# Performance work log

Hardware: AMD Instinct MI355X
Metric: run time of the kernel (lower is better)

## Reference

```python
import jax, jax.numpy as jnp
import numpy as np

D_MODEL = 1024
NUM_HEADS = 16
D_K = D_MODEL // NUM_HEADS
D_FF = 4096
B, S = 16, 512


def setup_inputs() -> dict:
    key = jax.random.key(0)
    ks = jax.random.split(key, 9)
    scale = 1.0 / np.sqrt(D_MODEL)
    inp = {
        "x": jax.random.normal(ks[0], (B, S, D_MODEL), dtype=jnp.float32),
        # attention projections, stored as [in, out] (apply as x @ W)
        "Wq": jax.random.normal(ks[1], (D_MODEL, D_MODEL), dtype=jnp.float32) * scale,
        "Wk": jax.random.normal(ks[2], (D_MODEL, D_MODEL), dtype=jnp.float32) * scale,
        "Wv": jax.random.normal(ks[3], (D_MODEL, D_MODEL), dtype=jnp.float32) * scale,
        "Wo": jax.random.normal(ks[4], (D_MODEL, D_MODEL), dtype=jnp.float32) * scale,
        # FFN
        "W1": jax.random.normal(ks[5], (D_MODEL, D_FF), dtype=jnp.float32) * scale,
        "b1": jnp.zeros((D_FF,), dtype=jnp.float32),
        "W2": jax.random.normal(ks[6], (D_FF, D_MODEL), dtype=jnp.float32) * (1.0 / np.sqrt(D_FF)),
        "b2": jnp.zeros((D_MODEL,), dtype=jnp.float32),
        # LayerNorms
        "g1": jnp.ones((D_MODEL,), dtype=jnp.float32),
        "be1": jnp.zeros((D_MODEL,), dtype=jnp.float32),
        "g2": jnp.ones((D_MODEL,), dtype=jnp.float32),
        "be2": jnp.zeros((D_MODEL,), dtype=jnp.float32),
    }
    return inp


def _layernorm(x, g, b, eps=1e-5):
    mu = jnp.mean(x, axis=-1, keepdims=True)
    var = jnp.mean(jnp.square(x - mu), axis=-1, keepdims=True)
    return (x - mu) * jax.lax.rsqrt(var + eps) * g + b


def _mha(x, Wq, Wk, Wv, Wo):
    b, s, _ = x.shape
    def split(h):  # [b,s,d] -> [b,H,s,dk]
        return h.reshape(b, s, NUM_HEADS, D_K).transpose(0, 2, 1, 3)
    Q, K, V = split(x @ Wq), split(x @ Wk), split(x @ Wv)
    scores = jnp.einsum("bhqd,bhkd->bhqk", Q, K) / np.sqrt(D_K)  # [b,H,s,s]
    causal = jnp.triu(jnp.ones((s, s), dtype=bool), k=1)
    scores = jnp.where(causal, -jnp.inf, scores)
    weights = jax.nn.softmax(scores, axis=-1)
    attn = jnp.einsum("bhqk,bhkd->bhqd", weights, V)
    attn = attn.transpose(0, 2, 1, 3).reshape(b, s, D_MODEL)
    return attn @ Wo


def reference(x, Wq, Wk, Wv, Wo, W1, b1, W2, b2, g1, be1, g2, be2):
    # pre-norm transformer block, dropout = 0 (eval)
    x = x + _mha(_layernorm(x, g1, be1), Wq, Wk, Wv, Wo)
    h = _layernorm(x, g2, be2)
    ffn = jax.nn.relu(h @ W1 + b1) @ W2 + b2
    return x + ffn
```

## Files before the change

### kernel.cpp

```cpp
#include <hip/hip_runtime.h>
#include <stdint.h>

#define NH 16
#define DK 64
#define BB 16
#define SS 512
#define DM 1024
#define DFF 4096

typedef __attribute__((ext_vector_type(8))) __bf16 bf16x8;
typedef __attribute__((ext_vector_type(4))) float  float4v;

__device__ __forceinline__ unsigned short f2bf(float f) {
  union { float f; unsigned int u; } v; v.f = f;
  unsigned int u = v.u + 0x7fffu + ((v.u >> 16) & 1u);
  return (unsigned short)(u >> 16);
}

__device__ __forceinline__ void gld_lds16(const void* g, void* l) {
  __builtin_amdgcn_global_load_lds(
      (const __attribute__((address_space(1))) unsigned int*)g,
      (__attribute__((address_space(3))) unsigned int*)l, 16, 0, 0);
}

__global__ void transpose_bf16(const float* __restrict__ in, unsigned short* __restrict__ out,
                               int R, int C) {
  __shared__ float tile[32][33];
  int c0 = blockIdx.x * 32, r0 = blockIdx.y * 32;
  int tx = threadIdx.x, ty = threadIdx.y;
  for (int j = ty; j < 32; j += 8)
    tile[j][tx] = in[(size_t)(r0 + j) * C + c0 + tx];
  __syncthreads();
  for (int j = ty; j < 32; j += 8)
    out[(size_t)(c0 + j) * R + r0 + tx] = f2bf(tile[tx][j]);
}

__global__ __launch_bounds__(256) void ln_bf16(const float* __restrict__ in,
                                               const float* __restrict__ g,
                                               const float* __restrict__ be,
                                               unsigned short* __restrict__ out) {
  int row = blockIdx.x, t = threadIdx.x;
  const float4* in4 = (const float4*)(in + (size_t)row * DM);
  float4 v = in4[t];
  float s  = v.x + v.y + v.z + v.w;
  float s2 = v.x * v.x + v.y * v.y + v.z * v.z + v.w * v.w;
  for (int off = 1; off < 64; off <<= 1) { s += __shfl_xor(s, off); s2 += __shfl_xor(s2, off); }
  __shared__ float rs[4], rs2[4];
  int wave = t >> 6;
  if ((t & 63) == 0) { rs[wave] = s; rs2[wave] = s2; }
  __syncthreads();
  s  = rs[0] + rs[1] + rs[2] + rs[3];
  s2 = rs2[0] + rs2[1] + rs2[2] + rs2[3];
  float mu = s * (1.f / DM);
  float var = s2 * (1.f / DM) - mu * mu;
  float rstd = rsqrtf(var + 1e-5f);
  float4 gv = ((const float4*)g)[t];
  float4 bv = ((const float4*)be)[t];
  unsigned short o0 = f2bf((v.x - mu) * rstd * gv.x + bv.x);
  unsigned short o1 = f2bf((v.y - mu) * rstd * gv.y + bv.y);
  unsigned short o2 = f2bf((v.z - mu) * rstd * gv.z + bv.z);
  unsigned short o3 = f2bf((v.w - mu) * rstd * gv.w + bv.w);
  uint2 pk; pk.x = o0 | ((unsigned)o1 << 16); pk.y = o2 | ((unsigned)o3 << 16);
  *(uint2*)(out + (size_t)row * DM + t * 4) = pk;
}

template <int MODE>
__global__ __launch_bounds__(256, 2)
void gemm_bt(const unsigned short* __restrict__ A, const unsigned short* __restrict__ Bt,
             int M, int N, int K,
             const float* __restrict__ bias, const float* __restrict__ resid,
             float* __restrict__ outf, unsigned short* __restrict__ outb,
             unsigned short* __restrict__ qo, unsigned short* __restrict__ ko,
             unsigned short* __restrict__ vo) {
  __shared__ __align__(16) unsigned short As[128 * 32];
  __shared__ __align__(16) unsigned short Bs[128 * 32];
  const int t = threadIdx.x, lane = t & 63, wave = t >> 6;
  const int lc = lane & 15, lr = lane >> 4;
  const int wm = wave >> 1, wn = wave & 1;
  const int rowblk = blockIdx.y * 128, colblk = blockIdx.x * 128;

  float4v acc[4][4];
#pragma unroll
  for (int i = 0; i < 4; i++)
#pragma unroll
    for (int j = 0; j < 4; j++) acc[i][j] = (float4v)0.f;

  const int r0 = t >> 2;
  const int k8 = (t & 3) * 8;

  for (int k0 = 0; k0 < K; k0 += 32) {
#pragma unroll
    for (int c = 0; c < 2; c++) {
      int row = c * 64 + r0;
      gld_lds16(A  + (size_t)(rowblk + row) * K + k0 + k8, &As[row * 32 + k8]);
      gld_lds16(Bt + (size_t)(colblk + row) * K + k0 + k8, &Bs[row * 32 + k8]);
    }
    __syncthreads();
    bf16x8 af[4], bfr[4];
#pragma unroll
    for (int mt = 0; mt < 4; mt++)
      af[mt] = *(const bf16x8*)&As[(wm * 64 + mt * 16 + lc) * 32 + lr * 8];
#pragma unroll
    for (int nt = 0; nt < 4; nt++)
      bfr[nt] = *(const bf16x8*)&Bs[(wn * 64 + nt * 16 + lc) * 32 + lr * 8];
#pragma unroll
    for (int mt = 0; mt < 4; mt++)
#pragma unroll
      for (int nt = 0; nt < 4; nt++)
        acc[mt][nt] = __builtin_amdgcn_mfma_f32_16x16x32_bf16(af[mt], bfr[nt], acc[mt][nt], 0, 0, 0);
    __syncthreads();
  }

#pragma unroll
  for (int mt = 0; mt < 4; mt++)
#pragma unroll
    for (int nt = 0; nt < 4; nt++)
#pragma unroll
      for (int r = 0; r < 4; r++) {
        int row = rowblk + wm * 64 + mt * 16 + lr * 4 + r;
        int col = colblk + wn * 64 + nt * 16 + lc;
        float v = acc[mt][nt][r];
        if (MODE == 0) {
          int b = row >> 9, s = row & 511;
          int f = col & 1023, h = f >> 6, d = f & 63;
          if (col < 1024)
            qo[(((size_t)b * NH + h) * SS + s) * DK + d] = f2bf(v);
          else if (col < 2048)
            ko[(((size_t)b * NH + h) * SS + s) * DK + d] = f2bf(v);
          else
            vo[(((size_t)b * NH + h) * DK + d) * SS + s] = f2bf(v);
        } else if (MODE == 1) {
          outf[(size_t)row * N + col] = resid[(size_t)row * N + col] + v;
        } else if (MODE == 2) {
          outb[(size_t)row * N + col] = f2bf(fmaxf(v + bias[col], 0.f));
        } else {
          outf[(size_t)row * N + col] = resid[(size_t)row * N + col] + v + bias[col];
        }
      }
}

__global__ __launch_bounds__(256, 2)
void attn(const unsigned short* __restrict__ Qb, const unsigned short* __restrict__ Kb,
          const unsigned short* __restrict__ Vtb, unsigned short* __restrict__ Ob) {
  __shared__ __align__(16) unsigned short Qs[128 * 64];
  __shared__ __align__(16) unsigned short Ks[128 * 64];
  __shared__ __align__(16) unsigned short Vts[64 * 128];
  __shared__ __align__(16) unsigned short Ps[4 * 32 * 128];
  const int t = threadIdx.x, lane = t & 63, wave = t >> 6;
  const int lc = lane & 15, lr = lane >> 4;
  const int qt = blockIdx.x, h = blockIdx.y, b = blockIdx.z;
  const int Q0 = qt * 128;
  const size_t headQK = ((size_t)b * NH + h) * SS * DK;
  const size_t headV  = ((size_t)b * NH + h) * DK * SS;
  const float SCALE = 0.125f, L2E = 1.44269504f;

  {
    const unsigned short* gq = Qb + headQK + (size_t)Q0 * DK;
#pragma unroll
    for (int c = 0; c < 4; c++)
      gld_lds16(gq + c * 2048 + t * 8, &Qs[c * 2048 + t * 8]);
  }

  float4v o_acc[2][4];
#pragma unroll
  for (int mt = 0; mt < 2; mt++)
#pragma unroll
    for (int nt = 0; nt < 4; nt++) o_acc[mt][nt] = (float4v)0.f;
  float m_i[2][4], l_i[2][4];
#pragma unroll
  for (int mt = 0; mt < 2; mt++)
#pragma unroll
    for (int r = 0; r < 4; r++) { m_i[mt][r] = -__builtin_inff(); l_i[mt][r] = 0.f; }

  for (int kt = 0; kt <= qt; kt++) {
    __syncthreads();
    const unsigned short* gk = Kb + headQK + (size_t)kt * 128 * DK;
#pragma unroll
    for (int c = 0; c < 4; c++)
      gld_lds16(gk + c * 2048 + t * 8, &Ks[c * 2048 + t * 8]);
#pragma unroll
    for (int c = 0; c < 4; c++) {
      int e = c * 2048 + t * 8;
      int d = e >> 7, cl = e & 127;
      gld_lds16(Vtb + headV + (size_t)d * SS + kt * 128 + cl, &Vts[e]);
    }
    __syncthreads();

    float4v s[2][8];
#pragma unroll
    for (int mt = 0; mt < 2; mt++)
#pragma unroll
      for (int nt = 0; nt < 8; nt++) s[mt][nt] = (float4v)0.f;
#pragma unroll
    for (int kk = 0; kk < 2; kk++) {
      bf16x8 aq[2];
#pragma unroll
      for (int mt = 0; mt < 2; mt++)
        aq[mt] = *(const bf16x8*)&Qs[(wave * 32 + mt * 16 + lc) * 64 + kk * 32 + lr * 8];
#pragma unroll
      for (int nt = 0; nt < 8; nt++) {
        bf16x8 bk = *(const bf16x8*)&Ks[(nt * 16 + lc) * 64 + kk * 32 + lr * 8];
#pragma unroll
        for (int mt = 0; mt < 2; mt++)
          s[mt][nt] = __builtin_amdgcn_mfma_f32_16x16x32_bf16(aq[mt], bk, s[mt][nt], 0, 0, 0);
      }
    }
    const bool diag = (kt == qt);
#pragma unroll
    for (int mt = 0; mt < 2; mt++)
#pragma unroll
      for (int nt = 0; nt < 8; nt++)
#pragma unroll
        for (int r = 0; r < 4; r++) {
          float sv = s[mt][nt][r] * SCALE;
          if (diag && (nt * 16 + lc > wave * 32 + mt * 16 + lr * 4 + r)) sv = -__builtin_inff();
          s[mt][nt][r] = sv;
        }
    float alpha_a[2][4];
#pragma unroll
    for (int mt = 0; mt < 2; mt++)
#pragma unroll
      for (int r = 0; r < 4; r++) {
        float mx = -__builtin_inff();
#pragma unroll
        for (int nt = 0; nt < 8; nt++) mx = fmaxf(mx, s[mt][nt][r]);
        for (int off = 1; off < 16; off <<= 1) mx = fmaxf(mx, __shfl_xor(mx, off));
        float mnew = fmaxf(m_i[mt][r], mx);
        float alpha = exp2f((m_i[mt][r] - mnew) * L2E);
        m_i[mt][r] = mnew;
        float rsum = 0.f;
#pragma unroll
        for (int nt = 0; nt < 8; nt++) {
          float p = exp2f((s[mt][nt][r] - mnew) * L2E);
          s[mt][nt][r] = p;
          rsum += p;
        }
        for (int off = 1; off < 16; off <<= 1) rsum += __shfl_xor(rsum, off);
        l_i[mt][r] = l_i[mt][r] * alpha + rsum;
        alpha_a[mt][r] = alpha;
      }
#pragma unroll
    for (int mt = 0; mt < 2; mt++)
#pragma unroll
      for (int nt = 0; nt < 4; nt++)
#pragma unroll
        for (int r = 0; r < 4; r++) o_acc[mt][nt][r] *= alpha_a[mt][r];
    const int wbase = wave * 32 * 128;
#pragma unroll
    for (int mt = 0; mt < 2; mt++)
#pragma unroll
      for (int nt = 0; nt < 8; nt++)
#pragma unroll
        for (int r = 0; r < 4; r++)
          Ps[wbase + (mt * 16 + lr * 4 + r) * 128 + nt * 16 + lc] = f2bf(s[mt][nt][r]);
#pragma unroll
    for (int kk = 0; kk < 4; kk++) {
      bf16x8 ap[2];
#pragma unroll
      for (int mt = 0; mt < 2; mt++)
        ap[mt] = *(const bf16x8*)&Ps[wbase + (mt * 16 + lc) * 128 + kk * 32 + lr * 8];
#pragma unroll
      for (int nt = 0; nt < 4; nt++) {
        bf16x8 bv = *(const bf16x8*)&Vts[(nt * 16 + lc) * 128 + kk * 32 + lr * 8];
#pragma unroll
        for (int mt = 0; mt < 2; mt++)
          o_acc[mt][nt] = __builtin_amdgcn_mfma_f32_16x16x32_bf16(ap[mt], bv, o_acc[mt][nt], 0, 0, 0);
      }
    }
  }
  float inv[2][4];
#pragma unroll
  for (int mt = 0; mt < 2; mt++)
#pragma unroll
    for (int r = 0; r < 4; r++) inv[mt][r] = 1.f / l_i[mt][r];
#pragma unroll
  for (int mt = 0; mt < 2; mt++)
#pragma unroll
    for (int nt = 0; nt < 4; nt++)
#pragma unroll
      for (int r = 0; r < 4; r++) {
        int sg = Q0 + wave * 32 + mt * 16 + lr * 4 + r;
        int col = h * DK + nt * 16 + lc;
        Ob[((size_t)b * SS + sg) * DM + col] = f2bf(o_acc[mt][nt][r] * inv[mt][r]);
      }
}

extern "C" void kernel_launch(void* const* d_in, const int* in_sizes, int n_in,
                              void* d_out, int out_size, void* d_ws, size_t ws_size,
                              hipStream_t stream) {
  const float* x  = (const float*)d_in[0];
  const float* Wq = (const float*)d_in[1];
  const float* Wk = (const float*)d_in[2];
  const float* Wv = (const float*)d_in[3];
  const float* Wo = (const float*)d_in[4];
  const float* W1 = (const float*)d_in[5];
  const float* b1 = (const float*)d_in[6];
  const float* W2 = (const float*)d_in[7];
  const float* b2 = (const float*)d_in[8];
  const float* g1 = (const float*)d_in[9];
  const float* be1 = (const float*)d_in[10];
  const float* g2 = (const float*)d_in[11];
  const float* be2 = (const float*)d_in[12];

  char* ws = (char*)d_ws;
  unsigned short* WqkvT = (unsigned short*)(ws);
  unsigned short* WoT   = (unsigned short*)(ws + 6291456);
  unsigned short* W1T   = (unsigned short*)(ws + 8388608);
  unsigned short* W2T   = (unsigned short*)(ws + 16777216);
  unsigned short* hbuf  = (unsigned short*)(ws + 25165824);
  unsigned short* Qb    = (unsigned short*)(ws + 41943040);
  unsigned short* Kb    = (unsigned short*)(ws + 58720256);
  unsigned short* Vtb   = (unsigned short*)(ws + 75497472);
  unsigned short* attnO = (unsigned short*)(ws + 92274688);
  float*          x1    = (float*)(ws + 109051904);
  unsigned short* ffn1  = (unsigned short*)(ws + 41943040);

  dim3 tb(32, 8);
  transpose_bf16<<<dim3(32, 32), tb, 0, stream>>>(Wq, WqkvT, 1024, 1024);
  transpose_bf16<<<dim3(32, 32), tb, 0, stream>>>(Wk, WqkvT + 1024 * 1024, 1024, 1024);
  transpose_bf16<<<dim3(32, 32), tb, 0, stream>>>(Wv, WqkvT + 2048 * 1024, 1024, 1024);
  transpose_bf16<<<dim3(32, 32), tb, 0, stream>>>(Wo, WoT, 1024, 1024);
  transpose_bf16<<<dim3(128, 32), tb, 0, stream>>>(W1, W1T, 1024, 4096);
  transpose_bf16<<<dim3(32, 128), tb, 0, stream>>>(W2, W2T, 4096, 1024);

  ln_bf16<<<8192, 256, 0, stream>>>(x, g1, be1, hbuf);

  gemm_bt<0><<<dim3(24, 64), 256, 0, stream>>>(hbuf, WqkvT, 8192, 3072, 1024,
      nullptr, nullptr, nullptr, nullptr, Qb, Kb, Vtb);

  attn<<<dim3(4, NH, BB), 256, 0, stream>>>(Qb, Kb, Vtb, attnO);

  gemm_bt<1><<<dim3(8, 64), 256, 0, stream>>>(attnO, WoT, 8192, 1024, 1024,
      nullptr, x, x1, nullptr, nullptr, nullptr, nullptr);

  ln_bf16<<<8192, 256, 0, stream>>>(x1, g2, be2, hbuf);

  gemm_bt<2><<<dim3(32, 64), 256, 0, stream>>>(hbuf, W1T, 8192, 4096, 1024,
      b1, nullptr, nullptr, ffn1, nullptr, nullptr, nullptr);

  gemm_bt<3><<<dim3(8, 64), 256, 0, stream>>>(ffn1, W2T, 8192, 1024, 4096,
      b2, x1, (float*)d_out, nullptr, nullptr, nullptr, nullptr);
}
```

Baseline: 559.4 us.

## Swizzle LDS layouts in GEMM and attention, group GEMM tiles, merge transposes

Applies XOR swizzling to the LDS tiles in the GEMM and attention kernels. Global addresses are permuted at load time and reads and writes use matching swizzled offsets, which is meant to avoid LDS bank conflicts on the 16-byte fragment reads and on the P-matrix stores. GEMM blocks are remapped into groups of 8 row tiles to improve L2 reuse. The six weight-transpose launches are merged into one kernel to cut launch overhead. The swizzle has to match exactly between loads and reads, or the results will be wrong.

```diff
diff --git a/kernel.cpp b/kernel.cpp
--- a/kernel.cpp
+++ b/kernel.cpp
@@ -23,10 +23,22 @@
       (__attribute__((address_space(3))) unsigned int*)l, 16, 0, 0);
 }
 
-__global__ void transpose_bf16(const float* __restrict__ in, unsigned short* __restrict__ out,
-                               int R, int C) {
+__global__ void transpose_all(const float* __restrict__ Wq, const float* __restrict__ Wk,
+                              const float* __restrict__ Wv, const float* __restrict__ Wo,
+                              const float* __restrict__ W1, const float* __restrict__ W2,
+                              unsigned short* __restrict__ WqkvT, unsigned short* __restrict__ WoT,
+                              unsigned short* __restrict__ W1T, unsigned short* __restrict__ W2T) {
   __shared__ float tile[32][33];
-  int c0 = blockIdx.x * 32, r0 = blockIdx.y * 32;
+  int bid = blockIdx.x;
+  const float* in; unsigned short* out; int R, C, tl;
+  if (bid < 1024)      { in = Wq; out = WqkvT;            R = 1024; C = 1024; tl = bid; }
+  else if (bid < 2048) { in = Wk; out = WqkvT + 1048576;  R = 1024; C = 1024; tl = bid - 1024; }
+  else if (bid < 3072) { in = Wv; out = WqkvT + 2097152;  R = 1024; C = 1024; tl = bid - 2048; }
+  else if (bid < 4096) { in = Wo; out = WoT;              R = 1024; C = 1024; tl = bid - 3072; }
+  else if (bid < 8192) { in = W1; out = W1T;              R = 1024; C = 4096; tl = bid - 4096; }
+  else                 { in = W2; out = W2T;              R = 4096; C = 1024; tl = bid - 8192; }
+  int ntx = C >> 5;
+  int c0 = (tl % ntx) * 32, r0 = (tl / ntx) * 32;
   int tx = threadIdx.x, ty = threadIdx.y;
   for (int j = ty; j < 32; j += 8)
     tile[j][tx] = in[(size_t)(r0 + j) * C + c0 + tx];
@@ -77,7 +89,14 @@
   const int t = threadIdx.x, lane = t & 63, wave = t >> 6;
   const int lc = lane & 15, lr = lane >> 4;
   const int wm = wave >> 1, wn = wave & 1;
-  const int rowblk = blockIdx.y * 128, colblk = blockIdx.x * 128;
+
+  const int nbn = gridDim.x;
+  int pid = blockIdx.y * nbn + blockIdx.x;
+  int nig = nbn << 3;
+  int gid = pid / nig;
+  int loc = pid - gid * nig;
+  const int rowblk = (gid * 8 + (loc & 7)) * 128;
+  const int colblk = (loc >> 3) * 128;
 
   float4v acc[4][4];
 #pragma unroll
@@ -86,23 +105,26 @@
     for (int j = 0; j < 4; j++) acc[i][j] = (float4v)0.f;
 
   const int r0 = t >> 2;
-  const int k8 = (t & 3) * 8;
+  const int sg = ((t & 3) ^ ((r0 >> 1) & 3));
+  const int ldsoff = r0 * 32 + (t & 3) * 8;
+  const int goff = sg * 8;
 
   for (int k0 = 0; k0 < K; k0 += 32) {
 #pragma unroll
     for (int c = 0; c < 2; c++) {
       int row = c * 64 + r0;
-      gld_lds16(A  + (size_t)(rowblk + row) * K + k0 + k8, &As[row * 32 + k8]);
-      gld_lds16(Bt + (size_t)(colblk + row) * K + k0 + k8, &Bs[row * 32 + k8]);
+      gld_lds16(A  + (size_t)(rowblk + row) * K + k0 + goff, &As[c * 2048 + ldsoff]);
+      gld_lds16(Bt + (size_t)(colblk + row) * K + k0 + goff, &Bs[c * 2048 + ldsoff]);
     }
     __syncthreads();
     bf16x8 af[4], bfr[4];
+    const int slot = (lr ^ ((lc >> 1) & 3)) * 8;
 #pragma unroll
     for (int mt = 0; mt < 4; mt++)
-      af[mt] = *(const bf16x8*)&As[(wm * 64 + mt * 16 + lc) * 32 + lr * 8];
+      af[mt] = *(const bf16x8*)&As[(wm * 64 + mt * 16 + lc) * 32 + slot];
 #pragma unroll
     for (int nt = 0; nt < 4; nt++)
-      bfr[nt] = *(const bf16x8*)&Bs[(wn * 64 + nt * 16 + lc) * 32 + lr * 8];
+      bfr[nt] = *(const bf16x8*)&Bs[(wn * 64 + nt * 16 + lc) * 32 + slot];
 #pragma unroll
     for (int mt = 0; mt < 4; mt++)
 #pragma unroll
@@ -154,11 +176,16 @@
   const size_t headV  = ((size_t)b * NH + h) * DK * SS;
   const float SCALE = 0.125f, L2E = 1.44269504f;
 
+  const int qkg = ((t & 7) ^ ((t >> 3) & 7)) * 8;
+  const int qkrow = (t >> 3) * 64;
+  const int vg = ((t & 15) ^ ((t >> 4) & 7)) * 8;
+  const int vrow = t >> 4;
+
   {
     const unsigned short* gq = Qb + headQK + (size_t)Q0 * DK;
 #pragma unroll
     for (int c = 0; c < 4; c++)
-      gld_lds16(gq + c * 2048 + t * 8, &Qs[c * 2048 + t * 8]);
+      gld_lds16(gq + c * 2048 + qkrow + qkg, &Qs[c * 2048 + t * 8]);
   }
 
   float4v o_acc[2][4];
@@ -177,12 +204,11 @@
     const unsigned short* gk = Kb + headQK + (size_t)kt * 128 * DK;
 #pragma unroll
     for (int c = 0; c < 4; c++)
-      gld_lds16(gk + c * 2048 + t * 8, &Ks[c * 2048 + t * 8]);
+      gld_lds16(gk + c * 2048 + qkrow + qkg, &Ks[c * 2048 + t * 8]);
 #pragma unroll
     for (int c = 0; c < 4; c++) {
-      int e = c * 2048 + t * 8;
-      int d = e >> 7, cl = e & 127;
-      gld_lds16(Vtb + headV + (size_t)d * SS + kt * 128 + cl, &Vts[e]);
+      int d = c * 16 + vrow;
+      gld_lds16(Vtb + headV + (size_t)d * SS + kt * 128 + vg, &Vts[c * 2048 + t * 8]);
     }
     __syncthreads();
 
@@ -195,11 +221,14 @@
     for (int kk = 0; kk < 2; kk++) {
       bf16x8 aq[2];
 #pragma unroll
-      for (int mt = 0; mt < 2; mt++)
-        aq[mt] = *(const bf16x8*)&Qs[(wave * 32 + mt * 16 + lc) * 64 + kk * 32 + lr * 8];
+      for (int mt = 0; mt < 2; mt++) {
+        int row = wave * 32 + mt * 16 + lc;
+        aq[mt] = *(const bf16x8*)&Qs[row * 64 + (((kk * 4 + lr) ^ (lc & 7)) * 8)];
+      }
 #pragma unroll
       for (int nt = 0; nt < 8; nt++) {
-        bf16x8 bk = *(const bf16x8*)&Ks[(nt * 16 + lc) * 64 + kk * 32 + lr * 8];
+        int row = nt * 16 + lc;
+        bf16x8 bk = *(const bf16x8*)&Ks[row * 64 + (((kk * 4 + lr) ^ (lc & 7)) * 8)];
 #pragma unroll
         for (int mt = 0; mt < 2; mt++)
           s[mt][nt] = __builtin_amdgcn_mfma_f32_16x16x32_bf16(aq[mt], bk, s[mt][nt], 0, 0, 0);
@@ -249,19 +278,26 @@
 #pragma unroll
     for (int mt = 0; mt < 2; mt++)
 #pragma unroll
-      for (int nt = 0; nt < 8; nt++)
-#pragma unroll
-        for (int r = 0; r < 4; r++)
-          Ps[wbase + (mt * 16 + lr * 4 + r) * 128 + nt * 16 + lc] = f2bf(s[mt][nt][r]);
+      for (int nt = 0; nt < 8; nt++) {
+        int g = nt * 2 + (lc >> 3);
+#pragma unroll
+        for (int r = 0; r < 4; r++) {
+          int rowp = mt * 16 + lr * 4 + r;
+          Ps[wbase + rowp * 128 + ((g ^ (rowp & 7)) * 8) + (lc & 7)] = f2bf(s[mt][nt][r]);
+        }
+      }
 #pragma unroll
     for (int kk = 0; kk < 4; kk++) {
       bf16x8 ap[2];
 #pragma unroll
-      for (int mt = 0; mt < 2; mt++)
-        ap[mt] = *(const bf16x8*)&Ps[wbase + (mt * 16 + lc) * 128 + kk * 32 + lr * 8];
+      for (int mt = 0; mt < 2; mt++) {
+        int rowp = mt * 16 + lc;
+        ap[mt] = *(const bf16x8*)&Ps[wbase + rowp * 128 + (((kk * 4 + lr) ^ (lc & 7)) * 8)];
+      }
 #pragma unroll
       for (int nt = 0; nt < 4; nt++) {
-        bf16x8 bv = *(const bf16x8*)&Vts[(nt * 16 + lc) * 128 + kk * 32 + lr * 8];
+        int row = nt * 16 + lc;
+        bf16x8 bv = *(const bf16x8*)&Vts[row * 128 + (((kk * 4 + lr) ^ (lc & 7)) * 8)];
 #pragma unroll
         for (int mt = 0; mt < 2; mt++)
           o_acc[mt][nt] = __builtin_amdgcn_mfma_f32_16x16x32_bf16(ap[mt], bv, o_acc[mt][nt], 0, 0, 0);
@@ -315,13 +351,8 @@
   float*          x1    = (float*)(ws + 109051904);
   unsigned short* ffn1  = (unsigned short*)(ws + 41943040);
 
-  dim3 tb(32, 8);
-  transpose_bf16<<<dim3(32, 32), tb, 0, stream>>>(Wq, WqkvT, 1024, 1024);
-  transpose_bf16<<<dim3(32, 32), tb, 0, stream>>>(Wk, WqkvT + 1024 * 1024, 1024, 1024);
-  transpose_bf16<<<dim3(32, 32), tb, 0, stream>>>(Wv, WqkvT + 2048 * 1024, 1024, 1024);
-  transpose_bf16<<<dim3(32, 32), tb, 0, stream>>>(Wo, WoT, 1024, 1024);
-  transpose_bf16<<<dim3(128, 32), tb, 0, stream>>>(W1, W1T, 1024, 4096);
-  transpose_bf16<<<dim3(32, 128), tb, 0, stream>>>(W2, W2T, 4096, 1024);
+  transpose_all<<<12288, dim3(32, 8), 0, stream>>>(Wq, Wk, Wv, Wo, W1, W2,
+                                                   WqkvT, WoT, W1T, W2T);
 
   ln_bf16<<<8192, 256, 0, stream>>>(x, g1, be1, hbuf);
 
```

After: 504.1 us. -9.9%, faster.
